# Kernel tuning notes

Measured on AMD Instinct MI355X. Metric: run time of the kernel, lower is better.

Reference implementation:

```python
import jax, jax.numpy as jnp
import numpy as np
from jax import lax

B, T, H, CTX, CONV_OUT = 32, 1536, 1024, 1024, 32


def setup_inputs() -> dict:
    key = jax.random.key(0)
    ks = jax.random.split(key, 10)
    s = 1.0 / np.sqrt(H)
    return {
        "decoder_output": jax.random.normal(ks[0], (B, 1, H), jnp.float32),
        "encoder_outputs": jax.random.normal(ks[1], (B, T, H), jnp.float32),
        "last_alignment": jax.random.uniform(ks[2], (B, T), jnp.float32),
        "W": jax.random.normal(ks[3], (CTX, H), jnp.float32) * s,
        "V": jax.random.normal(ks[4], (CTX, H), jnp.float32) * s,
        "U": jax.random.normal(ks[5], (CTX, CONV_OUT), jnp.float32) * (1.0 / np.sqrt(CONV_OUT)),
        "b": jax.random.uniform(ks[6], (CTX,), jnp.float32, -0.1, 0.1),
        "w": jax.random.normal(ks[7], (CTX,), jnp.float32) * (1.0 / np.sqrt(CTX)),
        "conv_w": jax.random.normal(ks[8], (CONV_OUT, 1, 3), jnp.float32) * 0.5,
        "conv_b": jax.random.normal(ks[9], (CONV_OUT,), jnp.float32) * 0.1,
    }


def reference(decoder_output, encoder_outputs, last_alignment, W, V, U, b, w, conv_w, conv_b):
    # location feature: Conv1d(1 -> conv_out, k=3, pad=1) over previous alignment
    conv = lax.conv_general_dilated(
        last_alignment[:, None, :], conv_w,
        window_strides=(1,), padding=[(1, 1)],
        dimension_numbers=("NCW", "OIW", "NCW"),
    ) + conv_b[None, :, None]                      # (B, conv_out, T)
    loc = jnp.transpose(conv, (0, 2, 1))           # (B, T, conv_out)

    # additive (Bahdanau) energies: (B,1,ctx) + (B,T,ctx) + (B,T,ctx) + (ctx,)
    e = jnp.tanh(
        jnp.einsum("bqh,ch->bqc", decoder_output, W)
        + jnp.einsum("bth,ch->btc", encoder_outputs, V)
        + jnp.einsum("btk,ck->btc", loc, U)
        + b
    )                                              # (B, T, ctx)
    scores = jnp.einsum("btc,c->bt", e, w)         # (B, T)
    alignment = jax.nn.softmax(scores, axis=-1)    # (B, T)
    context = jnp.einsum("bt,bth->bh", alignment, encoder_outputs)  # (B, H)
    return context, alignment
```

## Files before the change

### kernel.cpp

```cpp
#include <hip/hip_runtime.h>
#include <hip/hip_bf16.h>
#include <hip/hip_fp16.h>


constexpr int kB = 32, kT = 1536, kH = 1024, kC = 1024, kCO = 32;
constexpr int kM = kB * kT;
constexpr int kK = kH + kCO;

typedef _Float16 f16;
typedef _Float16 f16x8 __attribute__((ext_vector_type(8)));
typedef float f32x4 __attribute__((ext_vector_type(4)));

constexpr size_t WS_BF16  = 0;
constexpr size_t WS_LOC   = WS_BF16 + (size_t)kC * kK * 2;
constexpr size_t WS_ADD   = WS_LOC + (size_t)kM * kCO * 2;
constexpr size_t WS_SCORE = WS_ADD + (size_t)kB * kC * 4;
constexpr size_t WS_CTXP  = WS_SCORE + (size_t)4 * kM * 4;

__global__ void k_prep_b(const float* __restrict__ V, const float* __restrict__ U,
                         f16* __restrict__ Bf) {
    int idx = blockIdx.x * 256 + threadIdx.x;
    int c = idx / kK, k = idx - c * kK;
    float v = (k < kH) ? V[(size_t)c * kH + k] : U[(size_t)c * kCO + (k - kH)];
    Bf[idx] = (f16)v;
}

__global__ void k_prep_loc(const float* __restrict__ la, const float* __restrict__ cw,
                           const float* __restrict__ cb, f16* __restrict__ loc) {
    int m = blockIdx.x * 256 + threadIdx.x;
    int b = m / kT, t = m - b * kT;
    float x0 = (t > 0)      ? la[(size_t)b * kT + t - 1] : 0.f;
    float x1 = la[(size_t)b * kT + t];
    float x2 = (t < kT - 1) ? la[(size_t)b * kT + t + 1] : 0.f;
    union { f16 h[32]; int4 q[4]; } u;
#pragma unroll
    for (int k = 0; k < 32; ++k)
        u.h[k] = (f16)(cw[k * 3] * x0 + cw[k * 3 + 1] * x1 + cw[k * 3 + 2] * x2 + cb[k]);
    int4* dst = (int4*)(loc + (size_t)m * 32);
    dst[0] = u.q[0]; dst[1] = u.q[1]; dst[2] = u.q[2]; dst[3] = u.q[3];
}

__global__ void k_prep_add(const float* __restrict__ dec, const float* __restrict__ W,
                           const float* __restrict__ bias, float* __restrict__ add) {
    __shared__ float dl[kH];
    int bb = blockIdx.x >> 2;
    int cc = (blockIdx.x & 3) * 256 + threadIdx.x;
    *(float4*)&dl[threadIdx.x * 4] = *(const float4*)&dec[(size_t)bb * kH + threadIdx.x * 4];
    __syncthreads();
    float acc = bias[cc];
    const float* wr = W + (size_t)cc * kH;
    for (int h = 0; h < kH; h += 4) {
        float4 wv = *(const float4*)&wr[h];
        acc += wv.x * dl[h] + wv.y * dl[h + 1] + wv.z * dl[h + 2] + wv.w * dl[h + 3];
    }
    add[(size_t)bb * kC + cc] = acc;
}

__launch_bounds__(512)
__global__ void k_main(const float* __restrict__ enc, const f16* __restrict__ Bf,
                       const f16* __restrict__ loc, const float* __restrict__ add,
                       const float* __restrict__ wvec, float* __restrict__ spart) {
    __shared__ __align__(16) f16 As[128 * 64];
    __shared__ __align__(16) f16 Bs[256 * 64];
    __shared__ float add_l[256], w_l[256];
    __shared__ float sred[2][64][4];

    const int tid = threadIdx.x, lane = tid & 63, wave = tid >> 6;
    const int wm = wave >> 2, wn = wave & 3;
    const int mt = blockIdx.x >> 2, nt = blockIdx.x & 3;
    const int m0 = mt * 128, n0 = nt * 256;
    const int bb = m0 / kT;

    if (tid < 256) {
        add_l[tid] = add[(size_t)bb * kC + n0 + tid];
        w_l[tid]   = wvec[n0 + tid];
    }

    f32x4 acc[4][4];
#pragma unroll
    for (int i = 0; i < 4; ++i)
#pragma unroll
        for (int j = 0; j < 4; ++j) acc[i][j] = (f32x4){0.f, 0.f, 0.f, 0.f};

    const int ar = tid >> 2, aq = tid & 3;
    const int br = tid >> 1, bh = tid & 1;
    const float* ap = enc + (size_t)(m0 + ar) * kH + aq * 16;
    const f16*   bp = Bf + (size_t)(n0 + br) * kK;
    char* aw = (char*)As + ar * 128;
    char* bw = (char*)Bs + br * 128;
    const int axm = ar & 7, bxm = br & 7;

    for (int step = 0; step < 17; ++step) {
        if (step < 16) {
            const int k0 = step * 64;
            float4 f0 = *(const float4*)(ap + k0);
            float4 f1 = *(const float4*)(ap + k0 + 4);
            float4 f2 = *(const float4*)(ap + k0 + 8);
            float4 f3 = *(const float4*)(ap + k0 + 12);
            union { f16 h[16]; int4 q[2]; } pk;
            pk.h[0] = (f16)f0.x;  pk.h[1] = (f16)f0.y;  pk.h[2] = (f16)f0.z;  pk.h[3] = (f16)f0.w;
            pk.h[4] = (f16)f1.x;  pk.h[5] = (f16)f1.y;  pk.h[6] = (f16)f1.z;  pk.h[7] = (f16)f1.w;
            pk.h[8] = (f16)f2.x;  pk.h[9] = (f16)f2.y;  pk.h[10] = (f16)f2.z; pk.h[11] = (f16)f2.w;
            pk.h[12] = (f16)f3.x; pk.h[13] = (f16)f3.y; pk.h[14] = (f16)f3.z; pk.h[15] = (f16)f3.w;
            *(int4*)(aw + (((aq * 2 + 0) ^ axm) * 16)) = pk.q[0];
            *(int4*)(aw + (((aq * 2 + 1) ^ axm) * 16)) = pk.q[1];
            const char* bs = (const char*)(bp + k0 + bh * 32);
#pragma unroll
            for (int j = 0; j < 4; ++j) {
                int4 v = *(const int4*)(bs + j * 16);
                *(int4*)(bw + (((bh * 4 + j) ^ bxm) * 16)) = v;
            }
        } else {
            int4 v = *(const int4*)(loc + (size_t)(m0 + ar) * 32 + aq * 8);
            *(int4*)(aw + ((aq ^ axm) * 16)) = v;
#pragma unroll
            for (int j = 0; j < 2; ++j) {
                int4 w0 = *(const int4*)(bp + kH + (bh * 2 + j) * 8);
                *(int4*)(bw + (((bh * 2 + j) ^ bxm) * 16)) = w0;
            }
        }
        __syncthreads();
        const int nkk = (step < 16) ? 2 : 1;
        for (int kk = 0; kk < nkk; ++kk) {
            f16x8 af[4], bfr[4];
            const int g = lane >> 4, rl = lane & 15;
#pragma unroll
            for (int mi = 0; mi < 4; ++mi) {
                int row = wm * 64 + mi * 16 + rl;
                af[mi] = *(const f16x8*)((const char*)As + row * 128 + (((kk * 4 + g) ^ (row & 7)) * 16));
            }
#pragma unroll
            for (int ni = 0; ni < 4; ++ni) {
                int row = wn * 64 + ni * 16 + rl;
                bfr[ni] = *(const f16x8*)((const char*)Bs + row * 128 + (((kk * 4 + g) ^ (row & 7)) * 16));
            }
#pragma unroll
            for (int mi = 0; mi < 4; ++mi)
#pragma unroll
                for (int ni = 0; ni < 4; ++ni)
                    acc[mi][ni] = __builtin_amdgcn_mfma_f32_16x16x32_f16(af[mi], bfr[ni], acc[mi][ni], 0, 0, 0);
        }
        __syncthreads();
    }

#pragma unroll
    for (int mi = 0; mi < 4; ++mi) {
#pragma unroll
        for (int i = 0; i < 4; ++i) {
            float p = 0.f;
#pragma unroll
            for (int ni = 0; ni < 4; ++ni) {
                int cl = wn * 64 + ni * 16 + (lane & 15);
                float e = tanhf(acc[mi][ni][i] + add_l[cl]);
                p += e * w_l[cl];
            }
            p += __shfl_xor(p, 1);
            p += __shfl_xor(p, 2);
            p += __shfl_xor(p, 4);
            p += __shfl_xor(p, 8);
            if ((lane & 15) == 0)
                sred[wm][mi * 16 + (lane >> 4) * 4 + i][wn] = p;
        }
    }
    __syncthreads();
    if (tid < 128) {
        int r = tid & 63, w2 = tid >> 6;
        float s = sred[w2][r][0] + sred[w2][r][1] + sred[w2][r][2] + sred[w2][r][3];
        spart[(size_t)nt * kM + m0 + tid] = s;
    }
}

__global__ void k_softmax(const float* __restrict__ spart, float* __restrict__ out_align) {
    __shared__ float red[256];
    int b = blockIdx.x, tid = threadIdx.x;
    float v[6];
    float mx = -1e30f;
#pragma unroll
    for (int i = 0; i < 6; ++i) {
        size_t idx = (size_t)b * kT + tid + i * 256;
        float s = spart[idx] + spart[kM + idx] + spart[2 * (size_t)kM + idx] + spart[3 * (size_t)kM + idx];
        v[i] = s; mx = fmaxf(mx, s);
    }
    red[tid] = mx; __syncthreads();
    for (int o = 128; o > 0; o >>= 1) { if (tid < o) red[tid] = fmaxf(red[tid], red[tid + o]); __syncthreads(); }
    mx = red[0]; __syncthreads();
    float sum = 0.f;
#pragma unroll
    for (int i = 0; i < 6; ++i) { v[i] = expf(v[i] - mx); sum += v[i]; }
    red[tid] = sum; __syncthreads();
    for (int o = 128; o > 0; o >>= 1) { if (tid < o) red[tid] += red[tid + o]; __syncthreads(); }
    float inv = 1.f / red[0];
#pragma unroll
    for (int i = 0; i < 6; ++i)
        out_align[(size_t)b * kT + tid + i * 256] = v[i] * inv;
}

__global__ void k_ctx_part(const float* __restrict__ enc, const float* __restrict__ align,
                           float* __restrict__ cpart) {
    __shared__ float al[192];
    int ci = blockIdx.x, b = blockIdx.y, tid = threadIdx.x;
    if (tid < 192) al[tid] = align[(size_t)b * kT + ci * 192 + tid];
    __syncthreads();
    float4 acc = {0.f, 0.f, 0.f, 0.f};
    const float* ep = enc + ((size_t)b * kT + (size_t)ci * 192) * kH + tid * 4;
    for (int t = 0; t < 192; ++t) {
        float a = al[t];
        float4 e = *(const float4*)(ep + (size_t)t * kH);
        acc.x += a * e.x; acc.y += a * e.y; acc.z += a * e.z; acc.w += a * e.w;
    }
    *(float4*)&cpart[((size_t)ci * kB + b) * kH + tid * 4] = acc;
}

__global__ void k_ctx_red(const float* __restrict__ cpart, float* __restrict__ out_ctx) {
    int idx = blockIdx.x * 256 + threadIdx.x;
    float s = 0.f;
#pragma unroll
    for (int ci = 0; ci < 8; ++ci) s += cpart[(size_t)ci * kB * kH + idx];
    out_ctx[idx] = s;
}

extern "C" void kernel_launch(void* const* d_in, const int* in_sizes, int n_in,
                              void* d_out, int out_size, void* d_ws, size_t ws_size,
                              hipStream_t stream) {
    const float* dec  = (const float*)d_in[0];
    const float* enc  = (const float*)d_in[1];
    const float* la   = (const float*)d_in[2];
    const float* W    = (const float*)d_in[3];
    const float* V    = (const float*)d_in[4];
    const float* U    = (const float*)d_in[5];
    const float* bias = (const float*)d_in[6];
    const float* wv   = (const float*)d_in[7];
    const float* cw   = (const float*)d_in[8];
    const float* cb   = (const float*)d_in[9];

    char* ws = (char*)d_ws;
    f16* Bf      = (f16*)(ws + WS_BF16);
    f16* loc     = (f16*)(ws + WS_LOC);
    float* add   = (float*)(ws + WS_ADD);
    float* spart = (float*)(ws + WS_SCORE);
    float* cpart = (float*)(ws + WS_CTXP);

    float* out_ctx   = (float*)d_out;
    float* out_align = (float*)d_out + kB * kH;

    hipLaunchKernelGGL(k_prep_b,   dim3(kC * kK / 256), dim3(256), 0, stream, V, U, Bf);
    hipLaunchKernelGGL(k_prep_loc, dim3(kM / 256),      dim3(256), 0, stream, la, cw, cb, loc);
    hipLaunchKernelGGL(k_prep_add, dim3(kB * 4),        dim3(256), 0, stream, dec, W, bias, add);
    hipLaunchKernelGGL(k_main,     dim3((kM / 128) * 4), dim3(512), 0, stream, enc, Bf, loc, add, wv, spart);
    hipLaunchKernelGGL(k_softmax,  dim3(kB),            dim3(256), 0, stream, spart, out_align);
    hipLaunchKernelGGL(k_ctx_part, dim3(8, kB),         dim3(256), 0, stream, enc, out_align, cpart);
    hipLaunchKernelGGL(k_ctx_red,  dim3(kB * kH / 256), dim3(256), 0, stream, cpart, out_ctx);
}
```

Baseline: 234.7 us.

## Double-buffer LDS with register prefetch and 256-row tiles in main GEMM

Restructures the fused energy GEMM kernel to use 256x256 output tiles, with the A/B shared-memory tiles double-buffered. Global loads for the next K-slice are prefetched into registers while MFMAs run on the current slice, so there is one barrier per step. Block IDs are swizzled so that the four N-tiles sharing an encoder row block run close together for L2 reuse, and s_setprio raises priority around the MFMA bursts. The larger tile doubles the accumulator registers, and the launch bound hint of 2 blocks per CU with ~130KB LDS risks register spills or low occupancy.

New measurement: 273.7 us. +16.6%, slower.

```diff
diff --git a/kernel.cpp b/kernel.cpp
--- a/kernel.cpp
+++ b/kernel.cpp
@@ -56,19 +56,20 @@
     add[(size_t)bb * kC + cc] = acc;
 }
 
-__launch_bounds__(512)
+__launch_bounds__(512, 2)
 __global__ void k_main(const float* __restrict__ enc, const f16* __restrict__ Bf,
                        const f16* __restrict__ loc, const float* __restrict__ add,
                        const float* __restrict__ wvec, float* __restrict__ spart) {
-    __shared__ __align__(16) f16 As[128 * 64];
-    __shared__ __align__(16) f16 Bs[256 * 64];
-    __shared__ float add_l[256], w_l[256];
-    __shared__ float sred[2][64][4];
+    __shared__ __align__(16) char smem[133120];
+    float* add_l = (float*)(smem + 131072);
+    float* w_l   = (float*)(smem + 132096);
 
     const int tid = threadIdx.x, lane = tid & 63, wave = tid >> 6;
     const int wm = wave >> 2, wn = wave & 3;
-    const int mt = blockIdx.x >> 2, nt = blockIdx.x & 3;
-    const int m0 = mt * 128, n0 = nt * 256;
+    const int raw = blockIdx.x;
+    const int swz = (raw & 7) * 96 + (raw >> 3);
+    const int mt = swz >> 2, nt = swz & 3;
+    const int m0 = mt * 256, n0 = nt * 256;
     const int bb = m0 / kT;
 
     if (tid < 256) {
@@ -76,96 +77,157 @@
         w_l[tid]   = wvec[n0 + tid];
     }
 
-    f32x4 acc[4][4];
-#pragma unroll
-    for (int i = 0; i < 4; ++i)
+    f32x4 acc[8][4];
+#pragma unroll
+    for (int i = 0; i < 8; ++i)
 #pragma unroll
         for (int j = 0; j < 4; ++j) acc[i][j] = (f32x4){0.f, 0.f, 0.f, 0.f};
 
-    const int ar = tid >> 2, aq = tid & 3;
-    const int br = tid >> 1, bh = tid & 1;
-    const float* ap = enc + (size_t)(m0 + ar) * kH + aq * 16;
-    const f16*   bp = Bf + (size_t)(n0 + br) * kK;
-    char* aw = (char*)As + ar * 128;
-    char* bw = (char*)Bs + br * 128;
-    const int axm = ar & 7, bxm = br & 7;
-
-    for (int step = 0; step < 17; ++step) {
-        if (step < 16) {
-            const int k0 = step * 64;
-            float4 f0 = *(const float4*)(ap + k0);
-            float4 f1 = *(const float4*)(ap + k0 + 4);
-            float4 f2 = *(const float4*)(ap + k0 + 8);
-            float4 f3 = *(const float4*)(ap + k0 + 12);
-            union { f16 h[16]; int4 q[2]; } pk;
-            pk.h[0] = (f16)f0.x;  pk.h[1] = (f16)f0.y;  pk.h[2] = (f16)f0.z;  pk.h[3] = (f16)f0.w;
-            pk.h[4] = (f16)f1.x;  pk.h[5] = (f16)f1.y;  pk.h[6] = (f16)f1.z;  pk.h[7] = (f16)f1.w;
-            pk.h[8] = (f16)f2.x;  pk.h[9] = (f16)f2.y;  pk.h[10] = (f16)f2.z; pk.h[11] = (f16)f2.w;
-            pk.h[12] = (f16)f3.x; pk.h[13] = (f16)f3.y; pk.h[14] = (f16)f3.z; pk.h[15] = (f16)f3.w;
-            *(int4*)(aw + (((aq * 2 + 0) ^ axm) * 16)) = pk.q[0];
-            *(int4*)(aw + (((aq * 2 + 1) ^ axm) * 16)) = pk.q[1];
-            const char* bs = (const char*)(bp + k0 + bh * 32);
-#pragma unroll
-            for (int j = 0; j < 4; ++j) {
-                int4 v = *(const int4*)(bs + j * 16);
-                *(int4*)(bw + (((bh * 4 + j) ^ bxm) * 16)) = v;
-            }
+    const int srow = tid >> 1, shalf = tid & 1, sxm = srow & 7;
+    const float* a_src  = enc + (size_t)(m0 + srow) * kH + shalf * 32;
+    const f16*   b_src  = Bf  + (size_t)(n0 + srow) * kK + shalf * 32;
+    const f16*   l_src  = loc + (size_t)(m0 + srow) * kCO + shalf * 16;
+    const f16*   bt_src = Bf  + (size_t)(n0 + srow) * kK + kH + shalf * 16;
+
+    float4 a_ld[8]; int4 b_ld[4];
+    int4 ta0, ta1, tb0, tb1;
+
+#pragma unroll
+    for (int q = 0; q < 8; ++q) a_ld[q] = *(const float4*)(a_src + q * 4);
+#pragma unroll
+    for (int j = 0; j < 4; ++j) b_ld[j] = *(const int4*)(b_src + j * 8);
+    {
+        union { f16 h[32]; int4 q[4]; } pk;
+#pragma unroll
+        for (int q = 0; q < 8; ++q) {
+            pk.h[q * 4 + 0] = (f16)a_ld[q].x; pk.h[q * 4 + 1] = (f16)a_ld[q].y;
+            pk.h[q * 4 + 2] = (f16)a_ld[q].z; pk.h[q * 4 + 3] = (f16)a_ld[q].w;
+        }
+        char* Aw = smem + srow * 128;
+        char* Bw = smem + 65536 + srow * 128;
+#pragma unroll
+        for (int j = 0; j < 4; ++j) {
+            int sl = ((shalf * 4 + j) ^ sxm) * 16;
+            *(int4*)(Aw + sl) = pk.q[j];
+            *(int4*)(Bw + sl) = b_ld[j];
+        }
+    }
+    __syncthreads();
+
+    for (int t = 0; t < 16; ++t) {
+        const int cur = t & 1;
+        if (t < 15) {
+            const int k0 = (t + 1) * 64;
+#pragma unroll
+            for (int q = 0; q < 8; ++q) a_ld[q] = *(const float4*)(a_src + k0 + q * 4);
+#pragma unroll
+            for (int j = 0; j < 4; ++j) b_ld[j] = *(const int4*)(b_src + k0 + j * 8);
         } else {
-            int4 v = *(const int4*)(loc + (size_t)(m0 + ar) * 32 + aq * 8);
-            *(int4*)(aw + ((aq ^ axm) * 16)) = v;
-#pragma unroll
-            for (int j = 0; j < 2; ++j) {
-                int4 w0 = *(const int4*)(bp + kH + (bh * 2 + j) * 8);
-                *(int4*)(bw + (((bh * 2 + j) ^ bxm) * 16)) = w0;
-            }
-        }
-        __syncthreads();
-        const int nkk = (step < 16) ? 2 : 1;
-        for (int kk = 0; kk < nkk; ++kk) {
-            f16x8 af[4], bfr[4];
-            const int g = lane >> 4, rl = lane & 15;
-#pragma unroll
-            for (int mi = 0; mi < 4; ++mi) {
-                int row = wm * 64 + mi * 16 + rl;
-                af[mi] = *(const f16x8*)((const char*)As + row * 128 + (((kk * 4 + g) ^ (row & 7)) * 16));
+            ta0 = *(const int4*)(l_src);
+            ta1 = *(const int4*)(l_src + 8);
+            tb0 = *(const int4*)(bt_src);
+            tb1 = *(const int4*)(bt_src + 8);
+        }
+
+        const char* Ac = smem + cur * 32768;
+        const char* Bc = smem + 65536 + cur * 32768;
+        const int g = lane >> 4, rl = lane & 15;
+#pragma unroll
+        for (int kk = 0; kk < 2; ++kk) {
+            f16x8 af[8], bfv[4];
+#pragma unroll
+            for (int mi = 0; mi < 8; ++mi) {
+                int row = wm * 128 + mi * 16 + rl;
+                af[mi] = *(const f16x8*)(Ac + row * 128 + (((kk * 4 + g) ^ (row & 7)) * 16));
             }
 #pragma unroll
             for (int ni = 0; ni < 4; ++ni) {
                 int row = wn * 64 + ni * 16 + rl;
-                bfr[ni] = *(const f16x8*)((const char*)Bs + row * 128 + (((kk * 4 + g) ^ (row & 7)) * 16));
-            }
-#pragma unroll
-            for (int mi = 0; mi < 4; ++mi)
+                bfv[ni] = *(const f16x8*)(Bc + row * 128 + (((kk * 4 + g) ^ (row & 7)) * 16));
+            }
+            __builtin_amdgcn_s_setprio(1);
+#pragma unroll
+            for (int mi = 0; mi < 8; ++mi)
 #pragma unroll
                 for (int ni = 0; ni < 4; ++ni)
-                    acc[mi][ni] = __builtin_amdgcn_mfma_f32_16x16x32_f16(af[mi], bfr[ni], acc[mi][ni], 0, 0, 0);
+                    acc[mi][ni] = __builtin_amdgcn_mfma_f32_16x16x32_f16(af[mi], bfv[ni], acc[mi][ni], 0, 0, 0);
+            __builtin_amdgcn_s_setprio(0);
+        }
+
+        char* Aw = smem + (cur ^ 1) * 32768 + srow * 128;
+        char* Bw = smem + 65536 + (cur ^ 1) * 32768 + srow * 128;
+        if (t < 15) {
+            union { f16 h[32]; int4 q[4]; } pk;
+#pragma unroll
+            for (int q = 0; q < 8; ++q) {
+                pk.h[q * 4 + 0] = (f16)a_ld[q].x; pk.h[q * 4 + 1] = (f16)a_ld[q].y;
+                pk.h[q * 4 + 2] = (f16)a_ld[q].z; pk.h[q * 4 + 3] = (f16)a_ld[q].w;
+            }
+#pragma unroll
+            for (int j = 0; j < 4; ++j) {
+                int sl = ((shalf * 4 + j) ^ sxm) * 16;
+                *(int4*)(Aw + sl) = pk.q[j];
+                *(int4*)(Bw + sl) = b_ld[j];
+            }
+        } else {
+            *(int4*)(Aw + (((shalf * 2 + 0) ^ sxm) * 16)) = ta0;
+            *(int4*)(Aw + (((shalf * 2 + 1) ^ sxm) * 16)) = ta1;
+            *(int4*)(Bw + (((shalf * 2 + 0) ^ sxm) * 16)) = tb0;
+            *(int4*)(Bw + (((shalf * 2 + 1) ^ sxm) * 16)) = tb1;
         }
         __syncthreads();
     }
 
-#pragma unroll
-    for (int mi = 0; mi < 4; ++mi) {
-#pragma unroll
-        for (int i = 0; i < 4; ++i) {
-            float p = 0.f;
-#pragma unroll
-            for (int ni = 0; ni < 4; ++ni) {
-                int cl = wn * 64 + ni * 16 + (lane & 15);
-                float e = tanhf(acc[mi][ni][i] + add_l[cl]);
-                p += e * w_l[cl];
-            }
-            p += __shfl_xor(p, 1);
-            p += __shfl_xor(p, 2);
-            p += __shfl_xor(p, 4);
-            p += __shfl_xor(p, 8);
-            if ((lane & 15) == 0)
-                sred[wm][mi * 16 + (lane >> 4) * 4 + i][wn] = p;
+    {
+        const char* Ac = smem;
+        const char* Bc = smem + 65536;
+        const int g = lane >> 4, rl = lane & 15;
+        f16x8 af[8], bfv[4];
+#pragma unroll
+        for (int mi = 0; mi < 8; ++mi) {
+            int row = wm * 128 + mi * 16 + rl;
+            af[mi] = *(const f16x8*)(Ac + row * 128 + ((g ^ (row & 7)) * 16));
+        }
+#pragma unroll
+        for (int ni = 0; ni < 4; ++ni) {
+            int row = wn * 64 + ni * 16 + rl;
+            bfv[ni] = *(const f16x8*)(Bc + row * 128 + ((g ^ (row & 7)) * 16));
+        }
+        __builtin_amdgcn_s_setprio(1);
+#pragma unroll
+        for (int mi = 0; mi < 8; ++mi)
+#pragma unroll
+            for (int ni = 0; ni < 4; ++ni)
+                acc[mi][ni] = __builtin_amdgcn_mfma_f32_16x16x32_f16(af[mi], bfv[ni], acc[mi][ni], 0, 0, 0);
+        __builtin_amdgcn_s_setprio(0);
+    }
+
+    float (*sred)[128][4] = (float (*)[128][4])(smem + 98304);
+    {
+        const int rl = lane & 15, gq = lane >> 4;
+#pragma unroll
+        for (int mi = 0; mi < 8; ++mi) {
+#pragma unroll
+            for (int i = 0; i < 4; ++i) {
+                float p = 0.f;
+#pragma unroll
+                for (int ni = 0; ni < 4; ++ni) {
+                    int cl = wn * 64 + ni * 16 + rl;
+                    float e = tanhf(acc[mi][ni][i] + add_l[cl]);
+                    p += e * w_l[cl];
+                }
+                p += __shfl_xor(p, 1);
+                p += __shfl_xor(p, 2);
+                p += __shfl_xor(p, 4);
+                p += __shfl_xor(p, 8);
+                if (rl == 0) sred[wm][mi * 16 + gq * 4 + i][wn] = p;
+            }
         }
     }
     __syncthreads();
-    if (tid < 128) {
-        int r = tid & 63, w2 = tid >> 6;
-        float s = sred[w2][r][0] + sred[w2][r][1] + sred[w2][r][2] + sred[w2][r][3];
+    if (tid < 256) {
+        float s = sred[tid >> 7][tid & 127][0] + sred[tid >> 7][tid & 127][1]
+                + sred[tid >> 7][tid & 127][2] + sred[tid >> 7][tid & 127][3];
         spart[(size_t)nt * kM + m0 + tid] = s;
     }
 }
@@ -246,7 +308,7 @@
     hipLaunchKernelGGL(k_prep_b,   dim3(kC * kK / 256), dim3(256), 0, stream, V, U, Bf);
     hipLaunchKernelGGL(k_prep_loc, dim3(kM / 256),      dim3(256), 0, stream, la, cw, cb, loc);
     hipLaunchKernelGGL(k_prep_add, dim3(kB * 4),        dim3(256), 0, stream, dec, W, bias, add);
-    hipLaunchKernelGGL(k_main,     dim3((kM / 128) * 4), dim3(512), 0, stream, enc, Bf, loc, add, wv, spart);
+    hipLaunchKernelGGL(k_main,     dim3((kM / 256) * 4), dim3(512), 0, stream, enc, Bf, loc, add, wv, spart);
     hipLaunchKernelGGL(k_softmax,  dim3(kB),            dim3(256), 0, stream, spart, out_align);
     hipLaunchKernelGGL(k_ctx_part, dim3(8, kB),         dim3(256), 0, stream, enc, out_align, cpart);
     hipLaunchKernelGGL(k_ctx_red,  dim3(kB * kH / 256), dim3(256), 0, stream, cpart, out_ctx);
```

## Pre-convert encoder to fp16 padded matrix and use direct-to-LDS double-buffered GEMM

Applied to the files above, without the earlier changes.

Adds a pre-pass that converts encoder outputs to fp16 and packs them, together with the location features, into one padded K=1088 A matrix. The main GEMM then streams A and B tiles straight into LDS with global_load_lds, double-buffered, using 256x256 tiles, interleaved barriers with MFMA priority, and block-index swizzling for L2 locality. The aim is to remove in-loop fp32-to-fp16 conversion and register staging while overlapping loads with MFMA work. In exchange it costs an extra roughly 100MB fp16 write and read of the encoder and needs a large workspace; the old path stays as a fallback when the workspace is too small.

Result: slower. 266.2 us (+13.4%).

```diff
diff --git a/kernel.cpp b/kernel.cpp
--- a/kernel.cpp
+++ b/kernel.cpp
@@ -5,28 +5,46 @@
 
 constexpr int kB = 32, kT = 1536, kH = 1024, kC = 1024, kCO = 32;
 constexpr int kM = kB * kT;
-constexpr int kK = kH + kCO;
+constexpr int kKp = 1088;
+constexpr int kKf = 1056;
 
 typedef _Float16 f16;
 typedef _Float16 f16x8 __attribute__((ext_vector_type(8)));
 typedef float f32x4 __attribute__((ext_vector_type(4)));
 
-constexpr size_t WS_BF16  = 0;
-constexpr size_t WS_LOC   = WS_BF16 + (size_t)kC * kK * 2;
-constexpr size_t WS_ADD   = WS_LOC + (size_t)kM * kCO * 2;
-constexpr size_t WS_SCORE = WS_ADD + (size_t)kB * kC * 4;
-constexpr size_t WS_CTXP  = WS_SCORE + (size_t)4 * kM * 4;
-
-__global__ void k_prep_b(const float* __restrict__ V, const float* __restrict__ U,
-                         f16* __restrict__ Bf) {
-    int idx = blockIdx.x * 256 + threadIdx.x;
-    int c = idx / kK, k = idx - c * kK;
-    float v = (k < kH) ? V[(size_t)c * kH + k] : U[(size_t)c * kCO + (k - kH)];
-    Bf[idx] = (f16)v;
-}
-
-__global__ void k_prep_loc(const float* __restrict__ la, const float* __restrict__ cw,
-                           const float* __restrict__ cb, f16* __restrict__ loc) {
+constexpr size_t W2_A     = 0;
+constexpr size_t W2_B     = W2_A + (size_t)kM * kKp * 2;
+constexpr size_t W2_ADD   = W2_B + (size_t)kC * kKp * 2;
+constexpr size_t W2_SCORE = W2_ADD + (size_t)kB * kC * 4;
+constexpr size_t W2_CTXP  = W2_SCORE + (size_t)4 * kM * 4;
+constexpr size_t W2_NEED  = W2_CTXP + (size_t)8 * kB * kH * 4;
+
+constexpr size_t WF_B     = 0;
+constexpr size_t WF_LOC   = WF_B + (size_t)kC * kKf * 2;
+constexpr size_t WF_ADD   = WF_LOC + (size_t)kM * kCO * 2;
+constexpr size_t WF_SCORE = WF_ADD + (size_t)kB * kC * 4;
+constexpr size_t WF_CTXP  = WF_SCORE + (size_t)4 * kM * 4;
+
+__device__ __forceinline__ void gload16(const void* g, void* l) {
+    __builtin_amdgcn_global_load_lds(
+        (const __attribute__((address_space(1))) void*)g,
+        (__attribute__((address_space(3))) void*)l, 16, 0, 0);
+}
+
+__global__ void k_cvt(const float* __restrict__ enc, f16* __restrict__ Af) {
+    int gid = blockIdx.x * 256 + threadIdx.x;
+    int row = gid >> 7, c8 = gid & 127;
+    const float* src = enc + (size_t)row * kH + c8 * 8;
+    float4 e0 = *(const float4*)src;
+    float4 e1 = *(const float4*)(src + 4);
+    union { f16 h[8]; int4 q; } u;
+    u.h[0] = (f16)e0.x; u.h[1] = (f16)e0.y; u.h[2] = (f16)e0.z; u.h[3] = (f16)e0.w;
+    u.h[4] = (f16)e1.x; u.h[5] = (f16)e1.y; u.h[6] = (f16)e1.z; u.h[7] = (f16)e1.w;
+    *(int4*)(Af + (size_t)row * kKp + c8 * 8) = u.q;
+}
+
+__global__ void k_loc(const float* __restrict__ la, const float* __restrict__ cw,
+                      const float* __restrict__ cb, f16* __restrict__ Af) {
     int m = blockIdx.x * 256 + threadIdx.x;
     int b = m / kT, t = m - b * kT;
     float x0 = (t > 0)      ? la[(size_t)b * kT + t - 1] : 0.f;
@@ -36,8 +54,20 @@
 #pragma unroll
     for (int k = 0; k < 32; ++k)
         u.h[k] = (f16)(cw[k * 3] * x0 + cw[k * 3 + 1] * x1 + cw[k * 3 + 2] * x2 + cb[k]);
-    int4* dst = (int4*)(loc + (size_t)m * 32);
+    int4* dst = (int4*)(Af + (size_t)m * kKp + kH);
     dst[0] = u.q[0]; dst[1] = u.q[1]; dst[2] = u.q[2]; dst[3] = u.q[3];
+    int4 z = {0, 0, 0, 0};
+    dst[4] = z; dst[5] = z; dst[6] = z; dst[7] = z;
+}
+
+__global__ void k_prep_b2(const float* __restrict__ V, const float* __restrict__ U,
+                          f16* __restrict__ Bf) {
+    int c = blockIdx.x;
+    for (int k = threadIdx.x; k < kKp; k += 256) {
+        float v = (k < kH) ? V[(size_t)c * kH + k]
+                : (k < kH + kCO) ? U[(size_t)c * kCO + (k - kH)] : 0.f;
+        Bf[(size_t)c * kKp + k] = (f16)v;
+    }
 }
 
 __global__ void k_prep_add(const float* __restrict__ dec, const float* __restrict__ W,
@@ -56,10 +86,174 @@
     add[(size_t)bb * kC + cc] = acc;
 }
 
+#define RD_A2(x, MI) { const int row_ = wm * 128 + (MI) * 16 + rl;                            \
+    af[x][0] = *(const f16x8*)(Ac + row_ * 128 + (((0 + g) ^ (rl & 7)) * 16));                \
+    af[x][1] = *(const f16x8*)(Ac + row_ * 128 + (((4 + g) ^ (rl & 7)) * 16)); }
+
+#define MFMA_Q(Q)                                                                             \
+    __builtin_amdgcn_s_setprio(1);                                                            \
+    { _Pragma("unroll") for (int ni = 0; ni < 4; ++ni) {                                      \
+        acc[2*(Q)][ni]   = __builtin_amdgcn_mfma_f32_16x16x32_f16(af[0][0], bfv[ni][0], acc[2*(Q)][ni],   0, 0, 0); \
+        acc[2*(Q)][ni]   = __builtin_amdgcn_mfma_f32_16x16x32_f16(af[0][1], bfv[ni][1], acc[2*(Q)][ni],   0, 0, 0); \
+        acc[2*(Q)+1][ni] = __builtin_amdgcn_mfma_f32_16x16x32_f16(af[1][0], bfv[ni][0], acc[2*(Q)+1][ni], 0, 0, 0); \
+        acc[2*(Q)+1][ni] = __builtin_amdgcn_mfma_f32_16x16x32_f16(af[1][1], bfv[ni][1], acc[2*(Q)+1][ni], 0, 0, 0); } } \
+    __builtin_amdgcn_s_setprio(0);
+
+#define PBAR()                                                                                \
+    __builtin_amdgcn_s_barrier();                                                             \
+    asm volatile("s_waitcnt lgkmcnt(0)" ::: "memory");                                        \
+    __builtin_amdgcn_sched_barrier(0);
+
+__launch_bounds__(512, 2)
+__global__ void k_main(const f16* __restrict__ Ag, const f16* __restrict__ Bg,
+                       const float* __restrict__ add, const float* __restrict__ wvec,
+                       float* __restrict__ spart) {
+    __shared__ __align__(16) char smem[133120];
+    float* add_l = (float*)(smem + 131072);
+    float* w_l   = (float*)(smem + 132096);
+
+    const int tid = threadIdx.x, lane = tid & 63, wave = tid >> 6;
+    const int wm = wave >> 2, wn = wave & 3;
+    const int raw = blockIdx.x;
+    const int swz = (raw & 7) * 96 + (raw >> 3);
+    const int mt = swz >> 2, nt = swz & 3;
+    const int m0 = mt * 256, n0 = nt * 256;
+    const int bb = m0 / kT;
+
+    if (tid < 256) {
+        add_l[tid] = add[(size_t)bb * kC + n0 + tid];
+        w_l[tid]   = wvec[n0 + tid];
+    }
+
+    f32x4 acc[8][4];
+#pragma unroll
+    for (int i = 0; i < 8; ++i)
+#pragma unroll
+        for (int j = 0; j < 4; ++j) acc[i][j] = (f32x4){0.f, 0.f, 0.f, 0.f};
+
+    const int srow8 = lane >> 3;
+    const int sslot = (lane & 7) ^ srow8;
+    const f16* aSrc[4]; const f16* bSrc[4];
+#pragma unroll
+    for (int j = 0; j < 4; ++j) {
+        aSrc[j] = Ag + (size_t)(m0 + wave * 32 + j * 8 + srow8) * kKp + sslot * 8;
+        bSrc[j] = Bg + (size_t)(n0 + wave * 32 + j * 8 + srow8) * kKp + sslot * 8;
+    }
+    const int ldsOff = (wave * 32) * 128;
+
+#pragma unroll
+    for (int j = 0; j < 4; ++j) gload16(aSrc[j], smem + ldsOff + j * 1024);
+#pragma unroll
+    for (int j = 0; j < 4; ++j) gload16(bSrc[j], smem + 32768 + ldsOff + j * 1024);
+    asm volatile("s_waitcnt vmcnt(0) lgkmcnt(0)" ::: "memory");
+    __builtin_amdgcn_s_barrier();
+
+    const int g = lane >> 4, rl = lane & 15;
+
+    for (int t = 0; t < 17; ++t) {
+        const int cur = t & 1;
+        const char* Ac = smem + cur * 65536;
+        const char* Bc = smem + cur * 65536 + 32768;
+        char* An = smem + (cur ^ 1) * 65536 + ldsOff;
+        char* Bn = smem + (cur ^ 1) * 65536 + 32768 + ldsOff;
+        const size_t knxt = (size_t)(t + 1) * 64;
+
+        f16x8 bfv[4][2], af[2][2];
+
+        if (t < 16) {
+#pragma unroll
+            for (int j = 0; j < 4; ++j) gload16(aSrc[j] + knxt, An + j * 1024);
+        }
+#pragma unroll
+        for (int ni = 0; ni < 4; ++ni) {
+            const int row_ = wn * 64 + ni * 16 + rl;
+            bfv[ni][0] = *(const f16x8*)(Bc + row_ * 128 + (((0 + g) ^ (rl & 7)) * 16));
+            bfv[ni][1] = *(const f16x8*)(Bc + row_ * 128 + (((4 + g) ^ (rl & 7)) * 16));
+        }
+        RD_A2(0, 0) RD_A2(1, 1)
+        asm volatile("s_waitcnt lgkmcnt(8)" ::: "memory");
+        PBAR()
+        MFMA_Q(0)
+        __builtin_amdgcn_s_barrier();
+
+        if (t < 16) {
+#pragma unroll
+            for (int j = 0; j < 4; ++j) gload16(bSrc[j] + knxt, Bn + j * 1024);
+        }
+        RD_A2(0, 2) RD_A2(1, 3)
+        PBAR()
+        MFMA_Q(1)
+        __builtin_amdgcn_s_barrier();
+
+        RD_A2(0, 4) RD_A2(1, 5)
+        PBAR()
+        MFMA_Q(2)
+        __builtin_amdgcn_s_barrier();
+
+        RD_A2(0, 6) RD_A2(1, 7)
+        PBAR()
+        MFMA_Q(3)
+        asm volatile("s_waitcnt vmcnt(0)" ::: "memory");
+        __builtin_amdgcn_s_barrier();
+    }
+
+    float (*sred)[128][4] = (float (*)[128][4])(smem + 65536);
+    {
+        const int gq = lane >> 4;
+#pragma unroll
+        for (int mi = 0; mi < 8; ++mi) {
+#pragma unroll
+            for (int i = 0; i < 4; ++i) {
+                float p = 0.f;
+#pragma unroll
+                for (int ni = 0; ni < 4; ++ni) {
+                    int cl = wn * 64 + ni * 16 + rl;
+                    float e = tanhf(acc[mi][ni][i] + add_l[cl]);
+                    p += e * w_l[cl];
+                }
+                p += __shfl_xor(p, 1);
+                p += __shfl_xor(p, 2);
+                p += __shfl_xor(p, 4);
+                p += __shfl_xor(p, 8);
+                if (rl == 0) sred[wm][mi * 16 + gq * 4 + i][wn] = p;
+            }
+        }
+    }
+    __syncthreads();
+    if (tid < 256) {
+        float s = sred[tid >> 7][tid & 127][0] + sred[tid >> 7][tid & 127][1]
+                + sred[tid >> 7][tid & 127][2] + sred[tid >> 7][tid & 127][3];
+        spart[(size_t)nt * kM + m0 + tid] = s;
+    }
+}
+
+__global__ void k_prep_b_fb(const float* __restrict__ V, const float* __restrict__ U,
+                            f16* __restrict__ Bf) {
+    int idx = blockIdx.x * 256 + threadIdx.x;
+    int c = idx / kKf, k = idx - c * kKf;
+    float v = (k < kH) ? V[(size_t)c * kH + k] : U[(size_t)c * kCO + (k - kH)];
+    Bf[idx] = (f16)v;
+}
+
+__global__ void k_loc_fb(const float* __restrict__ la, const float* __restrict__ cw,
+                         const float* __restrict__ cb, f16* __restrict__ loc) {
+    int m = blockIdx.x * 256 + threadIdx.x;
+    int b = m / kT, t = m - b * kT;
+    float x0 = (t > 0)      ? la[(size_t)b * kT + t - 1] : 0.f;
+    float x1 = la[(size_t)b * kT + t];
+    float x2 = (t < kT - 1) ? la[(size_t)b * kT + t + 1] : 0.f;
+    union { f16 h[32]; int4 q[4]; } u;
+#pragma unroll
+    for (int k = 0; k < 32; ++k)
+        u.h[k] = (f16)(cw[k * 3] * x0 + cw[k * 3 + 1] * x1 + cw[k * 3 + 2] * x2 + cb[k]);
+    int4* dst = (int4*)(loc + (size_t)m * 32);
+    dst[0] = u.q[0]; dst[1] = u.q[1]; dst[2] = u.q[2]; dst[3] = u.q[3];
+}
+
 __launch_bounds__(512)
-__global__ void k_main(const float* __restrict__ enc, const f16* __restrict__ Bf,
-                       const f16* __restrict__ loc, const float* __restrict__ add,
-                       const float* __restrict__ wvec, float* __restrict__ spart) {
+__global__ void k_main_fb(const float* __restrict__ enc, const f16* __restrict__ Bf,
+                          const f16* __restrict__ loc, const float* __restrict__ add,
+                          const float* __restrict__ wvec, float* __restrict__ spart) {
     __shared__ __align__(16) f16 As[128 * 64];
     __shared__ __align__(16) f16 Bs[256 * 64];
     __shared__ float add_l[256], w_l[256];
@@ -85,7 +279,7 @@
     const int ar = tid >> 2, aq = tid & 3;
     const int br = tid >> 1, bh = tid & 1;
     const float* ap = enc + (size_t)(m0 + ar) * kH + aq * 16;
-    const f16*   bp = Bf + (size_t)(n0 + br) * kK;
+    const f16*   bp = Bf + (size_t)(n0 + br) * kKf;
     char* aw = (char*)As + ar * 128;
     char* bw = (char*)Bs + br * 128;
     const int axm = ar & 7, bxm = br & 7;
@@ -234,20 +428,37 @@
     const float* cb   = (const float*)d_in[9];
 
     char* ws = (char*)d_ws;
-    f16* Bf      = (f16*)(ws + WS_BF16);
-    f16* loc     = (f16*)(ws + WS_LOC);
-    float* add   = (float*)(ws + WS_ADD);
-    float* spart = (float*)(ws + WS_SCORE);
-    float* cpart = (float*)(ws + WS_CTXP);
-
     float* out_ctx   = (float*)d_out;
     float* out_align = (float*)d_out + kB * kH;
 
-    hipLaunchKernelGGL(k_prep_b,   dim3(kC * kK / 256), dim3(256), 0, stream, V, U, Bf);
-    hipLaunchKernelGGL(k_prep_loc, dim3(kM / 256),      dim3(256), 0, stream, la, cw, cb, loc);
-    hipLaunchKernelGGL(k_prep_add, dim3(kB * 4),        dim3(256), 0, stream, dec, W, bias, add);
-    hipLaunchKernelGGL(k_main,     dim3((kM / 128) * 4), dim3(512), 0, stream, enc, Bf, loc, add, wv, spart);
-    hipLaunchKernelGGL(k_softmax,  dim3(kB),            dim3(256), 0, stream, spart, out_align);
-    hipLaunchKernelGGL(k_ctx_part, dim3(8, kB),         dim3(256), 0, stream, enc, out_align, cpart);
-    hipLaunchKernelGGL(k_ctx_red,  dim3(kB * kH / 256), dim3(256), 0, stream, cpart, out_ctx);
-}
+    if (ws_size >= W2_NEED) {
+        f16* Af      = (f16*)(ws + W2_A);
+        f16* Bf      = (f16*)(ws + W2_B);
+        float* add   = (float*)(ws + W2_ADD);
+        float* spart = (float*)(ws + W2_SCORE);
+        float* cpart = (float*)(ws + W2_CTXP);
+
+        hipLaunchKernelGGL(k_prep_b2, dim3(kC),             dim3(256), 0, stream, V, U, Bf);
+        hipLaunchKernelGGL(k_loc,     dim3(kM / 256),       dim3(256), 0, stream, la, cw, cb, Af);
+        hipLaunchKernelGGL(k_cvt,     dim3(kM * kH / 8 / 256), dim3(256), 0, stream, enc, Af);
+        hipLaunchKernelGGL(k_prep_add, dim3(kB * 4),        dim3(256), 0, stream, dec, W, bias, add);
+        hipLaunchKernelGGL(k_main,    dim3((kM / 256) * 4), dim3(512), 0, stream, Af, Bf, add, wv, spart);
+        hipLaunchKernelGGL(k_softmax, dim3(kB),             dim3(256), 0, stream, spart, out_align);
+        hipLaunchKernelGGL(k_ctx_part, dim3(8, kB),         dim3(256), 0, stream, enc, out_align, cpart);
+        hipLaunchKernelGGL(k_ctx_red, dim3(kB * kH / 256),  dim3(256), 0, stream, cpart, out_ctx);
+    } else {
+        f16* Bf      = (f16*)(ws + WF_B);
+        f16* loc     = (f16*)(ws + WF_LOC);
+        float* add   = (float*)(ws + WF_ADD);
+        float* spart = (float*)(ws + WF_SCORE);
+        float* cpart = (float*)(ws + WF_CTXP);
+
+        hipLaunchKernelGGL(k_prep_b_fb, dim3(kC * kKf / 256), dim3(256), 0, stream, V, U, Bf);
+        hipLaunchKernelGGL(k_loc_fb,  dim3(kM / 256),       dim3(256), 0, stream, la, cw, cb, loc);
+        hipLaunchKernelGGL(k_prep_add, dim3(kB * 4),        dim3(256), 0, stream, dec, W, bias, add);
+        hipLaunchKernelGGL(k_main_fb, dim3((kM / 128) * 4), dim3(512), 0, stream, enc, Bf, loc, add, wv, spart);
+        hipLaunchKernelGGL(k_softmax, dim3(kB),             dim3(256), 0, stream, spart, out_align);
+        hipLaunchKernelGGL(k_ctx_part, dim3(8, kB),         dim3(256), 0, stream, enc, out_align, cpart);
+        hipLaunchKernelGGL(k_ctx_red, dim3(kB * kH / 256),  dim3(256), 0, stream, cpart, out_ctx);
+    }
+}
```

## Stage GEMM tiles via direct global-to-LDS loads with fp32 A converted at fragment read

Applied to the files above, without the earlier changes.

The main GEMM now loads encoder fp32 tiles and fp16 weight tiles straight into LDS with global_load_lds, using XOR-swizzled source addresses, instead of loading through registers and converting before the LDS store. The fp32-to-fp16 conversion of A moves to fragment read time, which doubles the A tile's LDS footprint. Blocks are remapped so that each group of eight consecutive block IDs is spread across the grid, and launch bounds request higher occupancy. The weight and location buffers are padded to 64-wide rows so the loc tail step fits the same load path. This adds LDS pressure and conversion work inside the MFMA loop, and the loop is still not double-buffered.

Result: faster. 221.3 us (-5.7%).

```diff
diff --git a/kernel.cpp b/kernel.cpp
--- a/kernel.cpp
+++ b/kernel.cpp
@@ -5,28 +5,36 @@
 
 constexpr int kB = 32, kT = 1536, kH = 1024, kC = 1024, kCO = 32;
 constexpr int kM = kB * kT;
-constexpr int kK = kH + kCO;
+constexpr int kKb = 1088;
 
 typedef _Float16 f16;
 typedef _Float16 f16x8 __attribute__((ext_vector_type(8)));
 typedef float f32x4 __attribute__((ext_vector_type(4)));
 
-constexpr size_t WS_BF16  = 0;
-constexpr size_t WS_LOC   = WS_BF16 + (size_t)kC * kK * 2;
-constexpr size_t WS_ADD   = WS_LOC + (size_t)kM * kCO * 2;
+constexpr size_t WS_B     = 0;
+constexpr size_t WS_LOC   = WS_B + (size_t)kC * kKb * 2;
+constexpr size_t WS_ADD   = WS_LOC + (size_t)kM * 64 * 2;
 constexpr size_t WS_SCORE = WS_ADD + (size_t)kB * kC * 4;
 constexpr size_t WS_CTXP  = WS_SCORE + (size_t)4 * kM * 4;
 
-__global__ void k_prep_b(const float* __restrict__ V, const float* __restrict__ U,
-                         f16* __restrict__ Bf) {
-    int idx = blockIdx.x * 256 + threadIdx.x;
-    int c = idx / kK, k = idx - c * kK;
-    float v = (k < kH) ? V[(size_t)c * kH + k] : U[(size_t)c * kCO + (k - kH)];
-    Bf[idx] = (f16)v;
-}
-
-__global__ void k_prep_loc(const float* __restrict__ la, const float* __restrict__ cw,
-                           const float* __restrict__ cb, f16* __restrict__ loc) {
+__device__ __forceinline__ void gload16(const void* g, void* l) {
+    __builtin_amdgcn_global_load_lds(
+        (const __attribute__((address_space(1))) void*)g,
+        (__attribute__((address_space(3))) void*)l, 16, 0, 0);
+}
+
+__global__ void k_prep_b2(const float* __restrict__ V, const float* __restrict__ U,
+                          f16* __restrict__ Bf) {
+    int c = blockIdx.x;
+    for (int k = threadIdx.x; k < kKb; k += 256) {
+        float v = (k < kH) ? V[(size_t)c * kH + k]
+                : (k < kH + kCO) ? U[(size_t)c * kCO + (k - kH)] : 0.f;
+        Bf[(size_t)c * kKb + k] = (f16)v;
+    }
+}
+
+__global__ void k_loc(const float* __restrict__ la, const float* __restrict__ cw,
+                      const float* __restrict__ cb, f16* __restrict__ locPad) {
     int m = blockIdx.x * 256 + threadIdx.x;
     int b = m / kT, t = m - b * kT;
     float x0 = (t > 0)      ? la[(size_t)b * kT + t - 1] : 0.f;
@@ -36,7 +44,7 @@
 #pragma unroll
     for (int k = 0; k < 32; ++k)
         u.h[k] = (f16)(cw[k * 3] * x0 + cw[k * 3 + 1] * x1 + cw[k * 3 + 2] * x2 + cb[k]);
-    int4* dst = (int4*)(loc + (size_t)m * 32);
+    int4* dst = (int4*)(locPad + (size_t)m * 64);
     dst[0] = u.q[0]; dst[1] = u.q[1]; dst[2] = u.q[2]; dst[3] = u.q[3];
 }
 
@@ -56,18 +64,20 @@
     add[(size_t)bb * kC + cc] = acc;
 }
 
-__launch_bounds__(512)
+__launch_bounds__(512, 4)
 __global__ void k_main(const float* __restrict__ enc, const f16* __restrict__ Bf,
-                       const f16* __restrict__ loc, const float* __restrict__ add,
+                       const f16* __restrict__ locPad, const float* __restrict__ add,
                        const float* __restrict__ wvec, float* __restrict__ spart) {
-    __shared__ __align__(16) f16 As[128 * 64];
-    __shared__ __align__(16) f16 Bs[256 * 64];
-    __shared__ float add_l[256], w_l[256];
-    __shared__ float sred[2][64][4];
+    __shared__ __align__(16) char smem[69632];
+    float* add_l = (float*)(smem + 65536);
+    float* w_l   = (float*)(smem + 66560);
+    float (*sred)[64][4] = (float (*)[64][4])(smem + 67584);
 
     const int tid = threadIdx.x, lane = tid & 63, wave = tid >> 6;
     const int wm = wave >> 2, wn = wave & 3;
-    const int mt = blockIdx.x >> 2, nt = blockIdx.x & 3;
+    const int raw = blockIdx.x;
+    const int lin = (raw & 7) * 192 + (raw >> 3);
+    const int mt = lin >> 2, nt = lin & 3;
     const int m0 = mt * 128, n0 = nt * 256;
     const int bb = m0 / kT;
 
@@ -82,63 +92,73 @@
 #pragma unroll
         for (int j = 0; j < 4; ++j) acc[i][j] = (f32x4){0.f, 0.f, 0.f, 0.f};
 
-    const int ar = tid >> 2, aq = tid & 3;
-    const int br = tid >> 1, bh = tid & 1;
-    const float* ap = enc + (size_t)(m0 + ar) * kH + aq * 16;
-    const f16*   bp = Bf + (size_t)(n0 + br) * kK;
-    char* aw = (char*)As + ar * 128;
-    char* bw = (char*)Bs + br * 128;
-    const int axm = ar & 7, bxm = br & 7;
-
-    for (int step = 0; step < 17; ++step) {
-        if (step < 16) {
-            const int k0 = step * 64;
-            float4 f0 = *(const float4*)(ap + k0);
-            float4 f1 = *(const float4*)(ap + k0 + 4);
-            float4 f2 = *(const float4*)(ap + k0 + 8);
-            float4 f3 = *(const float4*)(ap + k0 + 12);
-            union { f16 h[16]; int4 q[2]; } pk;
-            pk.h[0] = (f16)f0.x;  pk.h[1] = (f16)f0.y;  pk.h[2] = (f16)f0.z;  pk.h[3] = (f16)f0.w;
-            pk.h[4] = (f16)f1.x;  pk.h[5] = (f16)f1.y;  pk.h[6] = (f16)f1.z;  pk.h[7] = (f16)f1.w;
-            pk.h[8] = (f16)f2.x;  pk.h[9] = (f16)f2.y;  pk.h[10] = (f16)f2.z; pk.h[11] = (f16)f2.w;
-            pk.h[12] = (f16)f3.x; pk.h[13] = (f16)f3.y; pk.h[14] = (f16)f3.z; pk.h[15] = (f16)f3.w;
-            *(int4*)(aw + (((aq * 2 + 0) ^ axm) * 16)) = pk.q[0];
-            *(int4*)(aw + (((aq * 2 + 1) ^ axm) * 16)) = pk.q[1];
-            const char* bs = (const char*)(bp + k0 + bh * 32);
-#pragma unroll
-            for (int j = 0; j < 4; ++j) {
-                int4 v = *(const int4*)(bs + j * 16);
-                *(int4*)(bw + (((bh * 4 + j) ^ bxm) * 16)) = v;
-            }
-        } else {
-            int4 v = *(const int4*)(loc + (size_t)(m0 + ar) * 32 + aq * 8);
-            *(int4*)(aw + ((aq ^ axm) * 16)) = v;
-#pragma unroll
-            for (int j = 0; j < 2; ++j) {
-                int4 w0 = *(const int4*)(bp + kH + (bh * 2 + j) * 8);
-                *(int4*)(bw + (((bh * 2 + j) ^ bxm) * 16)) = w0;
+    const int rA = lane >> 4;
+    const float* aSrc[4];
+#pragma unroll
+    for (int j = 0; j < 4; ++j) {
+        int gc = (lane & 15) ^ ((j * 4 + rA) & 15);
+        aSrc[j] = enc + (size_t)(m0 + wave * 16 + j * 4 + rA) * kH + gc * 4;
+    }
+    const int rB = lane >> 3;
+    const int gcB = (lane & 7) ^ (rB & 7);
+    const f16* bSrc[4];
+#pragma unroll
+    for (int j = 0; j < 4; ++j)
+        bSrc[j] = Bf + (size_t)(n0 + wave * 32 + j * 8 + rB) * kKb + gcB * 8;
+
+    const unsigned aDst = wave * 4096u;
+    const unsigned bDst = 32768u + wave * 4096u;
+    const int g = lane >> 4, rl = lane & 15;
+
+    for (int t = 0; t < 16; ++t) {
+#pragma unroll
+        for (int j = 0; j < 4; ++j) gload16(aSrc[j] + t * 64, smem + aDst + j * 1024);
+#pragma unroll
+        for (int j = 0; j < 4; ++j) gload16(bSrc[j] + t * 64, smem + bDst + j * 1024);
+        __syncthreads();
+#pragma unroll
+        for (int kk = 0; kk < 2; ++kk) {
+            f16x8 bfv[4];
+#pragma unroll
+            for (int ni = 0; ni < 4; ++ni)
+                bfv[ni] = *(const f16x8*)(smem + 32768 + (wn * 64 + ni * 16 + rl) * 128
+                                          + (((kk * 4 + g) ^ (rl & 7)) << 4));
+#pragma unroll
+            for (int mi = 0; mi < 4; ++mi) {
+                const unsigned rowByte = (unsigned)((wm * 64 + mi * 16 + rl) * 256);
+                float4 lo = *(const float4*)(smem + rowByte + (((kk * 8 + 2 * g) ^ rl) << 4));
+                float4 hi = *(const float4*)(smem + rowByte + (((kk * 8 + 2 * g + 1) ^ rl) << 4));
+                f16x8 ah;
+                ah[0] = (f16)lo.x; ah[1] = (f16)lo.y; ah[2] = (f16)lo.z; ah[3] = (f16)lo.w;
+                ah[4] = (f16)hi.x; ah[5] = (f16)hi.y; ah[6] = (f16)hi.z; ah[7] = (f16)hi.w;
+#pragma unroll
+                for (int ni = 0; ni < 4; ++ni)
+                    acc[mi][ni] = __builtin_amdgcn_mfma_f32_16x16x32_f16(ah, bfv[ni], acc[mi][ni], 0, 0, 0);
             }
         }
         __syncthreads();
-        const int nkk = (step < 16) ? 2 : 1;
-        for (int kk = 0; kk < nkk; ++kk) {
-            f16x8 af[4], bfr[4];
-            const int g = lane >> 4, rl = lane & 15;
-#pragma unroll
-            for (int mi = 0; mi < 4; ++mi) {
-                int row = wm * 64 + mi * 16 + rl;
-                af[mi] = *(const f16x8*)((const char*)As + row * 128 + (((kk * 4 + g) ^ (row & 7)) * 16));
-            }
-#pragma unroll
-            for (int ni = 0; ni < 4; ++ni) {
-                int row = wn * 64 + ni * 16 + rl;
-                bfr[ni] = *(const f16x8*)((const char*)Bs + row * 128 + (((kk * 4 + g) ^ (row & 7)) * 16));
-            }
-#pragma unroll
-            for (int mi = 0; mi < 4; ++mi)
-#pragma unroll
-                for (int ni = 0; ni < 4; ++ni)
-                    acc[mi][ni] = __builtin_amdgcn_mfma_f32_16x16x32_f16(af[mi], bfr[ni], acc[mi][ni], 0, 0, 0);
+    }
+
+    {
+        const f16* tS0 = locPad + (size_t)(m0 + wave * 16 + 0 + rB) * 64 + gcB * 8;
+        const f16* tS1 = locPad + (size_t)(m0 + wave * 16 + 8 + rB) * 64 + gcB * 8;
+        gload16(tS0, smem + wave * 2048u);
+        gload16(tS1, smem + wave * 2048u + 1024u);
+#pragma unroll
+        for (int j = 0; j < 4; ++j) gload16(bSrc[j] + 1024, smem + bDst + j * 1024);
+        __syncthreads();
+        f16x8 bfv[4];
+#pragma unroll
+        for (int ni = 0; ni < 4; ++ni)
+            bfv[ni] = *(const f16x8*)(smem + 32768 + (wn * 64 + ni * 16 + rl) * 128
+                                      + ((g ^ (rl & 7)) << 4));
+#pragma unroll
+        for (int mi = 0; mi < 4; ++mi) {
+            f16x8 ah = *(const f16x8*)(smem + (wm * 64 + mi * 16 + rl) * 128
+                                       + ((g ^ (rl & 7)) << 4));
+#pragma unroll
+            for (int ni = 0; ni < 4; ++ni)
+                acc[mi][ni] = __builtin_amdgcn_mfma_f32_16x16x32_f16(ah, bfv[ni], acc[mi][ni], 0, 0, 0);
         }
         __syncthreads();
     }
@@ -150,7 +170,7 @@
             float p = 0.f;
 #pragma unroll
             for (int ni = 0; ni < 4; ++ni) {
-                int cl = wn * 64 + ni * 16 + (lane & 15);
+                int cl = wn * 64 + ni * 16 + rl;
                 float e = tanhf(acc[mi][ni][i] + add_l[cl]);
                 p += e * w_l[cl];
             }
@@ -158,8 +178,7 @@
             p += __shfl_xor(p, 2);
             p += __shfl_xor(p, 4);
             p += __shfl_xor(p, 8);
-            if ((lane & 15) == 0)
-                sred[wm][mi * 16 + (lane >> 4) * 4 + i][wn] = p;
+            if (rl == 0) sred[wm][mi * 16 + g * 4 + i][wn] = p;
         }
     }
     __syncthreads();
@@ -234,8 +253,8 @@
     const float* cb   = (const float*)d_in[9];
 
     char* ws = (char*)d_ws;
-    f16* Bf      = (f16*)(ws + WS_BF16);
-    f16* loc     = (f16*)(ws + WS_LOC);
+    f16* Bf      = (f16*)(ws + WS_B);
+    f16* locPad  = (f16*)(ws + WS_LOC);
     float* add   = (float*)(ws + WS_ADD);
     float* spart = (float*)(ws + WS_SCORE);
     float* cpart = (float*)(ws + WS_CTXP);
@@ -243,10 +262,10 @@
     float* out_ctx   = (float*)d_out;
     float* out_align = (float*)d_out + kB * kH;
 
-    hipLaunchKernelGGL(k_prep_b,   dim3(kC * kK / 256), dim3(256), 0, stream, V, U, Bf);
-    hipLaunchKernelGGL(k_prep_loc, dim3(kM / 256),      dim3(256), 0, stream, la, cw, cb, loc);
+    hipLaunchKernelGGL(k_prep_b2,  dim3(kC),            dim3(256), 0, stream, V, U, Bf);
+    hipLaunchKernelGGL(k_loc,      dim3(kM / 256),      dim3(256), 0, stream, la, cw, cb, locPad);
     hipLaunchKernelGGL(k_prep_add, dim3(kB * 4),        dim3(256), 0, stream, dec, W, bias, add);
-    hipLaunchKernelGGL(k_main,     dim3((kM / 128) * 4), dim3(512), 0, stream, enc, Bf, loc, add, wv, spart);
+    hipLaunchKernelGGL(k_main,     dim3((kM / 128) * 4), dim3(512), 0, stream, enc, Bf, locPad, add, wv, spart);
     hipLaunchKernelGGL(k_softmax,  dim3(kB),            dim3(256), 0, stream, spart, out_align);
     hipLaunchKernelGGL(k_ctx_part, dim3(8, kB),         dim3(256), 0, stream, enc, out_align, cpart);
     hipLaunchKernelGGL(k_ctx_red,  dim3(kB * kH / 256), dim3(256), 0, stream, cpart, out_ctx);
```
